# Kernel optimization log

Measured on AMD Instinct MI355X. Metric: run time of the kernel, lower is better.

## Reference

```python
import jax, jax.numpy as jnp
import numpy as np

T, B, IN_DIM = 2048, 8, 512
D_VALUE, D_KEY = 512, 128
CHUNK = 128
EPS = 1e-8


def setup_inputs() -> dict:
    key = jax.random.key(0)
    ks = jax.random.split(key, 9)
    s = 0.02
    return {
        "x": jax.random.normal(ks[0], (T, B, IN_DIM), dtype=jnp.float32),
        "Wv": jax.random.normal(ks[1], (D_VALUE, IN_DIM), dtype=jnp.float32) * s,
        "bv": jnp.zeros((D_VALUE,), dtype=jnp.float32),
        "Wk": jax.random.normal(ks[2], (D_KEY, IN_DIM), dtype=jnp.float32) * s,
        "bk": jnp.zeros((D_KEY,), dtype=jnp.float32),
        "Wq": jax.random.normal(ks[3], (D_KEY, IN_DIM), dtype=jnp.float32) * s,
        "bq": jnp.zeros((D_KEY,), dtype=jnp.float32),
        "Wa": jax.random.normal(ks[4], (D_KEY, IN_DIM), dtype=jnp.float32) * s,
        "ba": jnp.zeros((D_KEY,), dtype=jnp.float32),
    }


def _gla_forward(x, Wv, bv, Wk, bk, Wq, bq, Wa, ba):
    # Projections: x (T,B,in) -> v (T,B,d), k/q/alpha (T,B,n)
    v = jnp.einsum("tbi,di->tbd", x, Wv) + bv
    k = jnp.einsum("tbi,ni->tbn", x, Wk) + bk
    q = jnp.einsum("tbi,ni->tbn", x, Wq) + bq
    alpha = jax.nn.sigmoid(jnp.einsum("tbi,ni->tbn", x, Wa) + ba)

    Tt, Bb, d = v.shape
    n = k.shape[2]
    nch = Tt // CHUNK  # T chosen divisible by CHUNK

    # Reshape time-major tensors into (n_chunks, C, B, dim)
    v_r = v.reshape(nch, CHUNK, Bb, d)
    k_r = k.reshape(nch, CHUNK, Bb, n)
    q_r = q.reshape(nch, CHUNK, Bb, n)
    a_r = alpha.reshape(nch, CHUNK, Bb, n)

    def chunk_step(S_prev, inp):
        v_ch, k_ch, q_ch, a_ch = inp  # (C,B,d), (C,B,n), (C,B,n), (C,B,n)
        outer = jnp.einsum("tbd,tbn->tbdn", v_ch, k_ch)  # (C,B,d,n)
        cp = jnp.cumprod(jnp.maximum(a_ch, EPS), axis=0)  # (C,B,n)
        inv_prefix = 1.0 / (cp + EPS)
        scaled = jnp.cumsum(outer * inv_prefix[:, :, None, :], axis=0)
        # local decayed state plus carried state decayed by prefix product
        S_local = (scaled + S_prev[None, :, :, :]) * cp[:, :, None, :]
        y_ch = jnp.einsum("tbdn,tbn->tbd", S_local, q_ch)  # S @ q
        return S_local[-1], y_ch

    S0 = jnp.zeros((Bb, d, n), dtype=v.dtype)
    _, y = jax.lax.scan(chunk_step, S0, (v_r, k_r, q_r, a_r))
    return y.reshape(Tt, Bb, d)


def reference(x, Wv, bv, Wk, bk, Wq, bq, Wa, ba):
    return _gla_forward(x, Wv, bv, Wk, bk, Wq, bq, Wa, ba)
```

## Files before the change

kernel.cpp:

```cpp
#include <hip/hip_runtime.h>


#define EPSV 1e-8f

typedef __bf16 bf16x8 __attribute__((ext_vector_type(8)));
typedef float f32x4 __attribute__((ext_vector_type(4)));

__device__ __forceinline__ void async_copy16(const void* g, void* l) {
  __builtin_amdgcn_global_load_lds(
      (const __attribute__((address_space(1))) void*)g,
      (__attribute__((address_space(3))) void*)l, 16, 0, 0);
}

__global__ __launch_bounds__(256) void conv_bf16(const float* __restrict__ src,
                                                 __bf16* __restrict__ dst) {
  long i = ((long)blockIdx.x * 256 + threadIdx.x) * 8;
  float4 f0 = *(const float4*)(src + i);
  float4 f1 = *(const float4*)(src + i + 4);
  bf16x8 h;
  h[0] = (__bf16)f0.x; h[1] = (__bf16)f0.y; h[2] = (__bf16)f0.z; h[3] = (__bf16)f0.w;
  h[4] = (__bf16)f1.x; h[5] = (__bf16)f1.y; h[6] = (__bf16)f1.z; h[7] = (__bf16)f1.w;
  *(bf16x8*)(dst + i) = h;
}

__global__ __launch_bounds__(256) void conv_w(const float* __restrict__ Wv,
                                              const float* __restrict__ Wk,
                                              const float* __restrict__ Wq,
                                              const float* __restrict__ Wa,
                                              __bf16* __restrict__ dst) {
  long i = ((long)blockIdx.x * 256 + threadIdx.x) * 8;
  int row = (int)(i >> 9);
  int col = (int)(i & 511);
  const float* src;
  if (row < 512)      src = Wv + (long)row * 512 + col;
  else if (row < 640) src = Wk + (long)(row - 512) * 512 + col;
  else if (row < 768) src = Wq + (long)(row - 640) * 512 + col;
  else                src = Wa + (long)(row - 768) * 512 + col;
  float4 f0 = *(const float4*)(src);
  float4 f1 = *(const float4*)(src + 4);
  bf16x8 h;
  h[0] = (__bf16)f0.x; h[1] = (__bf16)f0.y; h[2] = (__bf16)f0.z; h[3] = (__bf16)f0.w;
  h[4] = (__bf16)f1.x; h[5] = (__bf16)f1.y; h[6] = (__bf16)f1.z; h[7] = (__bf16)f1.w;
  *(bf16x8*)(dst + i) = h;
}

__global__ __launch_bounds__(256) void proj_mfma(
    const __bf16* __restrict__ xb, const __bf16* __restrict__ wcat,
    const float* __restrict__ bv, const float* __restrict__ bk,
    const float* __restrict__ bq, const float* __restrict__ ba,
    __bf16* __restrict__ vt, __bf16* __restrict__ kout,
    __bf16* __restrict__ qout, float* __restrict__ aout) {
  __shared__ __attribute__((aligned(16))) char smem[128 * 136 * 2];
  __bf16* a_sm = (__bf16*)smem;
  __bf16* b_sm = a_sm + 128 * 32;
  __bf16* tr   = (__bf16*)smem;

  int tid = threadIdx.x;
  int lane = tid & 63, wave = tid >> 6;
  int mt = blockIdx.x, nt = blockIdx.y;
  int wr = wave >> 1, wcol = wave & 1;

  const __bf16* xtile = xb + (long)mt * 128 * 512;
  const __bf16* wtile = wcat + (long)nt * 128 * 512;

  f32x4 acc[4][4] = {};
  int lr = lane >> 2, lc = lane & 3;
  int l15 = lane & 15, qd = lane >> 4;

  for (int k0 = 0; k0 < 512; k0 += 32) {
#pragma unroll
    for (int h = 0; h < 2; ++h) {
      int q = wave * 2 + h;
      int row = q * 16 + lr;
      async_copy16(xtile + (long)row * 512 + k0 + lc * 8, &a_sm[q * 512]);
      async_copy16(wtile + (long)row * 512 + k0 + lc * 8, &b_sm[q * 512]);
    }
    __syncthreads();
    bf16x8 af[4], bfr[4];
#pragma unroll
    for (int t = 0; t < 4; ++t) {
      af[t]  = *(const bf16x8*)&a_sm[(wr * 64 + t * 16 + l15) * 32 + qd * 8];
      bfr[t] = *(const bf16x8*)&b_sm[(wcol * 64 + t * 16 + l15) * 32 + qd * 8];
    }
#pragma unroll
    for (int i = 0; i < 4; ++i)
#pragma unroll
      for (int j = 0; j < 4; ++j)
        acc[i][j] = __builtin_amdgcn_mfma_f32_16x16x32_bf16(af[i], bfr[j], acc[i][j], 0, 0, 0);
    __syncthreads();
  }

  if (nt < 4) {
    const float* bias = bv + nt * 128;
#pragma unroll
    for (int i = 0; i < 4; ++i)
#pragma unroll
      for (int j = 0; j < 4; ++j) {
        int col = wcol * 64 + j * 16 + l15;
        float bz = bias[col];
#pragma unroll
        for (int r = 0; r < 4; ++r) {
          int row = wr * 64 + i * 16 + qd * 4 + r;
          tr[col * 136 + (row & 7) * 16 + (row >> 3)] = (__bf16)(acc[i][j][r] + bz);
        }
      }
    __syncthreads();
    int cbase = (mt >> 3) * 8;
    int s0 = (mt & 7) * 16;
#pragma unroll
    for (int it = 0; it < 4; ++it) {
      int p = it * 256 + tid;
      int d = p & 127, b = p >> 7;
      bf16x8 u0 = *(const bf16x8*)&tr[d * 136 + b * 16];
      bf16x8 u1 = *(const bf16x8*)&tr[d * 136 + b * 16 + 8];
      __bf16* dst = vt + ((long)(cbase + b) * 512 + nt * 128 + d) * 128 + s0;
      *(bf16x8*)dst = u0;
      *(bf16x8*)(dst + 8) = u1;
    }
    return;
  }

  const float* bias; bool sig = false;
  __bf16* dstb = nullptr; float* dstf = nullptr;
  if (nt == 4)      { bias = bk; dstb = kout; }
  else if (nt == 5) { bias = bq; dstb = qout; }
  else              { bias = ba; dstf = aout; sig = true; }

#pragma unroll
  for (int i = 0; i < 4; ++i)
#pragma unroll
    for (int j = 0; j < 4; ++j) {
      int col = wcol * 64 + j * 16 + l15;
      float bz = bias[col];
#pragma unroll
      for (int r = 0; r < 4; ++r) {
        int row = wr * 64 + i * 16 + qd * 4 + r;
        float z = acc[i][j][r] + bz;
        long addr = ((long)mt * 128 + row) * 128 + col;
        if (sig) dstf[addr] = 1.f / (1.f + __expf(-z));
        else     dstb[addr] = (__bf16)z;
      }
    }
}

__global__ __launch_bounds__(256) void scan_cp(const float* __restrict__ a,
                                               const __bf16* __restrict__ k,
                                               const __bf16* __restrict__ q,
                                               __bf16* __restrict__ kbs,
                                               __bf16* __restrict__ qb,
                                               __bf16* __restrict__ kt,
                                               float* __restrict__ cpend) {
  int idx = blockIdx.x * 256 + threadIdx.x;
  int n = idx & 127;
  int b = (idx >> 7) & 7;
  int c = idx >> 10;
  long base = ((long)c * 1024 + b) * 128 + n;
  float cp = 1.f;
  __bf16 ktbuf[128];
#pragma unroll
  for (int tt = 0; tt < 128; ++tt) {
    long off = base + (long)tt * 1024;
    float av = fmaxf(a[off], EPSV);
    cp *= av;
    float kk = (float)k[off] / (cp + EPSV);
    float qq = (float)q[off] * cp;
    __bf16 kh = (__bf16)kk;
    kbs[off] = kh;
    qb[off] = (__bf16)qq;
    ktbuf[tt] = kh;
  }
  cpend[(c * 8 + b) * 128 + n] = cp;
  __bf16* dst = kt + ((long)((c * 8 + b) * 128 + n)) * 128;
#pragma unroll
  for (int i = 0; i < 16; ++i) {
    bf16x8 h;
#pragma unroll
    for (int j = 0; j < 8; ++j) h[j] = ktbuf[i * 8 + j];
    *(bf16x8*)(dst + i * 8) = h;
  }
}

__global__ __launch_bounds__(256) void gmm(const __bf16* __restrict__ vt,
                                           const __bf16* __restrict__ kt,
                                           const float* __restrict__ cpend,
                                           __bf16* __restrict__ Gt) {
  int tid = threadIdx.x, lane = tid & 63, wave = tid >> 6;
  int wr = wave >> 1, wc = wave & 1;
  int l15 = lane & 15, qd = lane >> 4;
  int cb = blockIdx.x >> 2, dt = blockIdx.x & 3;
  const __bf16* vbase = vt + ((long)cb * 512 + dt * 128) * 128;
  const __bf16* kbase = kt + (long)cb * 16384;
  f32x4 acc[4][4] = {};
#pragma unroll
  for (int kk = 0; kk < 4; ++kk) {
    int k0 = kk * 32;
    bf16x8 af[4], bfr[4];
#pragma unroll
    for (int i = 0; i < 4; ++i)
      af[i] = *(const bf16x8*)(vbase + (long)(wr * 64 + i * 16 + l15) * 128 + k0 + qd * 8);
#pragma unroll
    for (int j = 0; j < 4; ++j)
      bfr[j] = *(const bf16x8*)(kbase + (long)(wc * 64 + j * 16 + l15) * 128 + k0 + qd * 8);
#pragma unroll
    for (int i = 0; i < 4; ++i)
#pragma unroll
      for (int j = 0; j < 4; ++j)
        acc[i][j] = __builtin_amdgcn_mfma_f32_16x16x32_bf16(af[i], bfr[j], acc[i][j], 0, 0, 0);
  }
  float ce[4];
#pragma unroll
  for (int j = 0; j < 4; ++j) ce[j] = cpend[cb * 128 + wc * 64 + j * 16 + l15];
#pragma unroll
  for (int i = 0; i < 4; ++i)
#pragma unroll
    for (int j = 0; j < 4; ++j) {
      int col = wc * 64 + j * 16 + l15;
#pragma unroll
      for (int r = 0; r < 4; ++r) {
        int row = wr * 64 + i * 16 + qd * 4 + r;
        Gt[((long)cb * 512 + dt * 128 + row) * 128 + col] = (__bf16)(acc[i][j][r] * ce[j]);
      }
    }
}

__global__ __launch_bounds__(256) void scan_state(const __bf16* __restrict__ Gt,
                                                  const float* __restrict__ cpend,
                                                  __bf16* __restrict__ St) {
  long e = (long)blockIdx.x * 256 + threadIdx.x;
  int n = (int)(e & 127);
  int b = (int)(e >> 16);
  float S = 0.f;
#pragma unroll
  for (int c = 0; c < 16; ++c) {
    long idx = (long)c * 524288 + e;
    float g = (float)Gt[idx];
    St[idx] = (__bf16)S;
    S = g + S * cpend[(c * 8 + b) * 128 + n];
  }
}

__global__ __launch_bounds__(256) void ymm(const __bf16* __restrict__ qb,
                                           const __bf16* __restrict__ kbs,
                                           const __bf16* __restrict__ vt,
                                           const __bf16* __restrict__ St,
                                           float* __restrict__ out) {
  __shared__ __bf16 A_lds[128 * 136];
  int tid = threadIdx.x, lane = tid & 63, wave = tid >> 6;
  int wr = wave >> 1, wc = wave & 1;
  int l15 = lane & 15, qd = lane >> 4;
  int cb = blockIdx.x >> 2, dt = blockIdx.x & 3;
  int c = cb >> 3, b = cb & 7;
  const __bf16* qbase = qb + ((long)c * 1024 + b) * 128;
  const __bf16* kbase = kbs + ((long)c * 1024 + b) * 128;

  {
    f32x4 accA[4][4] = {};
#pragma unroll
    for (int kk = 0; kk < 4; ++kk) {
      int k0 = kk * 32;
      bf16x8 af[4], bfr[4];
#pragma unroll
      for (int i = 0; i < 4; ++i)
        af[i] = *(const bf16x8*)(qbase + (long)(wr * 64 + i * 16 + l15) * 1024 + k0 + qd * 8);
#pragma unroll
      for (int j = 0; j < 4; ++j)
        bfr[j] = *(const bf16x8*)(kbase + (long)(wc * 64 + j * 16 + l15) * 1024 + k0 + qd * 8);
#pragma unroll
      for (int i = 0; i < 4; ++i)
#pragma unroll
        for (int j = 0; j < 4; ++j)
          accA[i][j] = __builtin_amdgcn_mfma_f32_16x16x32_bf16(af[i], bfr[j], accA[i][j], 0, 0, 0);
    }
#pragma unroll
    for (int i = 0; i < 4; ++i)
#pragma unroll
      for (int j = 0; j < 4; ++j) {
        int s = wc * 64 + j * 16 + l15;
#pragma unroll
        for (int r = 0; r < 4; ++r) {
          int t = wr * 64 + i * 16 + qd * 4 + r;
          A_lds[t * 136 + s] = (s <= t) ? (__bf16)accA[i][j][r] : (__bf16)0.f;
        }
      }
  }
  __syncthreads();

  f32x4 acc[4][4] = {};
  const __bf16* vbase = vt + ((long)cb * 512 + dt * 128) * 128;
  const __bf16* sbase = St + ((long)cb * 512 + dt * 128) * 128;
#pragma unroll
  for (int kk = 0; kk < 4; ++kk) {
    int k0 = kk * 32;
    bf16x8 af[4], bfr[4];
#pragma unroll
    for (int i = 0; i < 4; ++i)
      af[i] = *(const bf16x8*)(vbase + (long)(wr * 64 + i * 16 + l15) * 128 + k0 + qd * 8);
#pragma unroll
    for (int j = 0; j < 4; ++j)
      bfr[j] = *(const bf16x8*)&A_lds[(wc * 64 + j * 16 + l15) * 136 + k0 + qd * 8];
#pragma unroll
    for (int i = 0; i < 4; ++i)
#pragma unroll
      for (int j = 0; j < 4; ++j)
        acc[i][j] = __builtin_amdgcn_mfma_f32_16x16x32_bf16(af[i], bfr[j], acc[i][j], 0, 0, 0);
  }
#pragma unroll
  for (int kk = 0; kk < 4; ++kk) {
    int k0 = kk * 32;
    bf16x8 af[4], bfr[4];
#pragma unroll
    for (int i = 0; i < 4; ++i)
      af[i] = *(const bf16x8*)(sbase + (long)(wr * 64 + i * 16 + l15) * 128 + k0 + qd * 8);
#pragma unroll
    for (int j = 0; j < 4; ++j)
      bfr[j] = *(const bf16x8*)(qbase + (long)(wc * 64 + j * 16 + l15) * 1024 + k0 + qd * 8);
#pragma unroll
    for (int i = 0; i < 4; ++i)
#pragma unroll
      for (int j = 0; j < 4; ++j)
        acc[i][j] = __builtin_amdgcn_mfma_f32_16x16x32_bf16(af[i], bfr[j], acc[i][j], 0, 0, 0);
  }

#pragma unroll
  for (int i = 0; i < 4; ++i)
#pragma unroll
    for (int j = 0; j < 4; ++j) {
      int colt = wc * 64 + j * 16 + l15;
      long addr = ((long)(c * 128 + colt) * 8 + b) * 512 + dt * 128 + wr * 64 + i * 16 + qd * 4;
      *(float4*)(out + addr) = *(float4*)&acc[i][j];
    }
}

extern "C" void kernel_launch(void* const* d_in, const int* in_sizes, int n_in,
                              void* d_out, int out_size, void* d_ws, size_t ws_size,
                              hipStream_t stream) {
  const float* x  = (const float*)d_in[0];
  const float* Wv = (const float*)d_in[1];
  const float* bv = (const float*)d_in[2];
  const float* Wk = (const float*)d_in[3];
  const float* bk = (const float*)d_in[4];
  const float* Wq = (const float*)d_in[5];
  const float* bq = (const float*)d_in[6];
  const float* Wa = (const float*)d_in[7];
  const float* ba = (const float*)d_in[8];
  float* out = (float*)d_out;
  float* ws = (float*)d_ws;

  float*  a_buf = ws;
  __bf16* qb    = (__bf16*)(ws + 2097152);
  __bf16* kbs   = (__bf16*)(ws + 3145728);
  __bf16* kt    = (__bf16*)(ws + 4194304);
  __bf16* vt    = (__bf16*)(ws + 5242880);
  __bf16* k_raw = (__bf16*)(ws + 9437184);
  __bf16* q_raw = (__bf16*)(ws + 10485760);
  __bf16* xb    = (__bf16*)(ws + 11534336);
  __bf16* Wcat  = (__bf16*)(ws + 15728640);
  __bf16* Gt    = xb;
  __bf16* St    = (__bf16*)(ws + 15958016);
  float*  cpend = ws + 20152320;

  conv_bf16<<<4096, 256, 0, stream>>>(x, xb);
  conv_w<<<224, 256, 0, stream>>>(Wv, Wk, Wq, Wa, Wcat);
  proj_mfma<<<dim3(128, 7), 256, 0, stream>>>(xb, Wcat, bv, bk, bq, ba,
                                              vt, k_raw, q_raw, a_buf);
  scan_cp<<<64, 256, 0, stream>>>(a_buf, k_raw, q_raw, kbs, qb, kt, cpend);
  gmm<<<512, 256, 0, stream>>>(vt, kt, cpend, Gt);
  scan_state<<<2048, 256, 0, stream>>>(Gt, cpend, St);
  ymm<<<512, 256, 0, stream>>>(qb, kbs, vt, St, out);
}
```

Before: 200.4 us.

## Swizzle projection LDS tiles, spread chunk scan over more blocks, vectorize state scan

The projection GEMM now XOR-swizzles the 16-byte chunks of the LDS tiles on store and on fragment load, to cut LDS bank conflicts. The cumprod scan launches 256 blocks of 64 threads instead of 64 blocks of 256, spreading its serial per-thread loop over more compute units. The inter-chunk state scan has each thread handle four contiguous elements with vector loads and stores, using a quarter of the blocks. These are three separate tweaks, and the swizzle has to match exactly between the async copy and the fragment reads.

```diff
diff --git a/kernel.cpp b/kernel.cpp
--- a/kernel.cpp
+++ b/kernel.cpp
@@ -4,6 +4,7 @@
 #define EPSV 1e-8f
 
 typedef __bf16 bf16x8 __attribute__((ext_vector_type(8)));
+typedef __bf16 bf16x4 __attribute__((ext_vector_type(4)));
 typedef float f32x4 __attribute__((ext_vector_type(4)));
 
 __device__ __forceinline__ void async_copy16(const void* g, void* l) {
@@ -66,21 +67,23 @@
   f32x4 acc[4][4] = {};
   int lr = lane >> 2, lc = lane & 3;
   int l15 = lane & 15, qd = lane >> 4;
+  int slsrc = (lc ^ ((lr >> 1) & 3)) * 8;
+  int frd = (l15 >> 1) & 3;
 
   for (int k0 = 0; k0 < 512; k0 += 32) {
 #pragma unroll
     for (int h = 0; h < 2; ++h) {
       int q = wave * 2 + h;
       int row = q * 16 + lr;
-      async_copy16(xtile + (long)row * 512 + k0 + lc * 8, &a_sm[q * 512]);
-      async_copy16(wtile + (long)row * 512 + k0 + lc * 8, &b_sm[q * 512]);
+      async_copy16(xtile + (long)row * 512 + k0 + slsrc, &a_sm[q * 512]);
+      async_copy16(wtile + (long)row * 512 + k0 + slsrc, &b_sm[q * 512]);
     }
     __syncthreads();
     bf16x8 af[4], bfr[4];
 #pragma unroll
     for (int t = 0; t < 4; ++t) {
-      af[t]  = *(const bf16x8*)&a_sm[(wr * 64 + t * 16 + l15) * 32 + qd * 8];
-      bfr[t] = *(const bf16x8*)&b_sm[(wcol * 64 + t * 16 + l15) * 32 + qd * 8];
+      af[t]  = *(const bf16x8*)&a_sm[(wr * 64 + t * 16 + l15) * 32 + (qd ^ frd) * 8];
+      bfr[t] = *(const bf16x8*)&b_sm[(wcol * 64 + t * 16 + l15) * 32 + (qd ^ frd) * 8];
     }
 #pragma unroll
     for (int i = 0; i < 4; ++i)
@@ -143,14 +146,14 @@
     }
 }
 
-__global__ __launch_bounds__(256) void scan_cp(const float* __restrict__ a,
-                                               const __bf16* __restrict__ k,
-                                               const __bf16* __restrict__ q,
-                                               __bf16* __restrict__ kbs,
-                                               __bf16* __restrict__ qb,
-                                               __bf16* __restrict__ kt,
-                                               float* __restrict__ cpend) {
-  int idx = blockIdx.x * 256 + threadIdx.x;
+__global__ __launch_bounds__(64) void scan_cp(const float* __restrict__ a,
+                                              const __bf16* __restrict__ k,
+                                              const __bf16* __restrict__ q,
+                                              __bf16* __restrict__ kbs,
+                                              __bf16* __restrict__ qb,
+                                              __bf16* __restrict__ kt,
+                                              float* __restrict__ cpend) {
+  int idx = blockIdx.x * 64 + threadIdx.x;
   int n = idx & 127;
   int b = (idx >> 7) & 7;
   int c = idx >> 10;
@@ -226,16 +229,23 @@
 __global__ __launch_bounds__(256) void scan_state(const __bf16* __restrict__ Gt,
                                                   const float* __restrict__ cpend,
                                                   __bf16* __restrict__ St) {
-  long e = (long)blockIdx.x * 256 + threadIdx.x;
-  int n = (int)(e & 127);
+  long e = ((long)blockIdx.x * 256 + threadIdx.x) * 4;
+  int n0 = (int)(e & 127);
   int b = (int)(e >> 16);
-  float S = 0.f;
+  float4 S = {0.f, 0.f, 0.f, 0.f};
 #pragma unroll
   for (int c = 0; c < 16; ++c) {
     long idx = (long)c * 524288 + e;
-    float g = (float)Gt[idx];
-    St[idx] = (__bf16)S;
-    S = g + S * cpend[(c * 8 + b) * 128 + n];
+    bf16x4 g = *(const bf16x4*)(Gt + idx);
+    bf16x4 sv;
+    sv[0] = (__bf16)S.x; sv[1] = (__bf16)S.y;
+    sv[2] = (__bf16)S.z; sv[3] = (__bf16)S.w;
+    *(bf16x4*)(St + idx) = sv;
+    const float4 cp = *(const float4*)(cpend + (c * 8 + b) * 128 + n0);
+    S.x = (float)g[0] + S.x * cp.x;
+    S.y = (float)g[1] + S.y * cp.y;
+    S.z = (float)g[2] + S.z * cp.z;
+    S.w = (float)g[3] + S.w * cp.w;
   }
 }
 
@@ -363,8 +373,8 @@
   conv_w<<<224, 256, 0, stream>>>(Wv, Wk, Wq, Wa, Wcat);
   proj_mfma<<<dim3(128, 7), 256, 0, stream>>>(xb, Wcat, bv, bk, bq, ba,
                                               vt, k_raw, q_raw, a_buf);
-  scan_cp<<<64, 256, 0, stream>>>(a_buf, k_raw, q_raw, kbs, qb, kt, cpend);
+  scan_cp<<<256, 64, 0, stream>>>(a_buf, k_raw, q_raw, kbs, qb, kt, cpend);
   gmm<<<512, 256, 0, stream>>>(vt, kt, cpend, Gt);
-  scan_state<<<2048, 256, 0, stream>>>(Gt, cpend, St);
+  scan_state<<<512, 256, 0, stream>>>(Gt, cpend, St);
   ymm<<<512, 256, 0, stream>>>(qb, kbs, vt, St, out);
 }
```

Result: slower. 204.6 us (+2.1%).
